# Kernel optimization log

Measured on AMD Instinct MI355X. Metric: run time of the kernel, lower is better.

## Reference

```python
import jax, jax.numpy as jnp
import numpy as np

N, E, G, H, IN = 50000, 500000, 64, 128, 5
BN_EPS = 1e-5


def setup_inputs() -> dict:
    key = jax.random.key(0)
    ks = jax.random.split(key, 12)
    x = jax.random.normal(ks[0], (N, IN), dtype=jnp.float32)
    edge_index = jax.random.randint(ks[1], (2, E), 0, N, dtype=jnp.int64)
    edge_attr = jax.random.uniform(ks[2], (E,), dtype=jnp.float32)
    batch = jnp.sort(jax.random.randint(ks[3], (N,), 0, G, dtype=jnp.int64))
    conv0_w = jax.random.normal(ks[4], (IN, H), dtype=jnp.float32) / np.sqrt(IN)
    conv0_b = jnp.zeros((H,), jnp.float32)
    conv_ws = jax.random.normal(ks[5], (3, H, H), dtype=jnp.float32) / np.sqrt(H)
    conv_bs = jnp.zeros((3, H), jnp.float32)
    bn_gamma = jnp.ones((4, H), jnp.float32)
    bn_beta = jnp.zeros((4, H), jnp.float32)
    fc1_w = jax.random.normal(ks[6], (H, 64), dtype=jnp.float32) / np.sqrt(H)
    fc1_b = jnp.zeros((64,), jnp.float32)
    fc2_w = jax.random.normal(ks[7], (64, 1), dtype=jnp.float32) / np.sqrt(64)
    fc2_b = jnp.zeros((1,), jnp.float32)
    return dict(x=x, edge_index=edge_index, edge_attr=edge_attr, batch=batch,
                num_graphs=G, conv0_w=conv0_w, conv0_b=conv0_b, conv_ws=conv_ws,
                conv_bs=conv_bs, bn_gamma=bn_gamma, bn_beta=bn_beta,
                fc1_w=fc1_w, fc1_b=fc1_b, fc2_w=fc2_w, fc2_b=fc2_b)


def reference(x, edge_index, edge_attr, batch, num_graphs, conv0_w, conv0_b,
              conv_ws, conv_bs, bn_gamma, bn_beta, fc1_w, fc1_b, fc2_w, fc2_b):
    n = x.shape[0]
    row, col = edge_index[0], edge_index[1]
    # PyG gcn_norm: add self-loops (weight 1), symmetric D^-1/2 A D^-1/2
    loops = jnp.arange(n)
    row_f = jnp.concatenate([row, loops])
    col_f = jnp.concatenate([col, loops])
    ew = jnp.concatenate([edge_attr, jnp.ones((n,), x.dtype)])
    deg = jax.ops.segment_sum(ew, col_f, num_segments=n)
    dinv = jnp.where(deg > 0, jax.lax.rsqrt(jnp.where(deg > 0, deg, 1.0)), 0.0)
    norm = dinv[row_f] * ew * dinv[col_f]  # [E+N]

    def gcn_conv(h, W, b):
        m = h @ W  # transform first, as in PyG GCNConv
        agg = jax.ops.segment_sum(norm[:, None] * m[row_f], col_f, num_segments=n)
        return agg + b

    def bn(h, g, bta):  # training-mode BatchNorm1d, biased variance
        mu = h.mean(axis=0)
        var = jnp.mean((h - mu) ** 2, axis=0)
        return g * (h - mu) * jax.lax.rsqrt(var + BN_EPS) + bta

    h = jax.nn.silu(bn(gcn_conv(x, conv0_w, conv0_b), bn_gamma[0], bn_beta[0]))
    for i in range(3):
        h = jax.nn.silu(bn(gcn_conv(h, conv_ws[i], conv_bs[i]),
                           bn_gamma[i + 1], bn_beta[i + 1]))

    # global_mean_pool over graph ids
    sums = jax.ops.segment_sum(h, batch, num_segments=num_graphs)
    counts = jax.ops.segment_sum(jnp.ones((n,), h.dtype), batch, num_segments=num_graphs)
    pooled = sums / jnp.maximum(counts, 1.0)[:, None]

    out = jax.nn.silu(pooled @ fc1_w + fc1_b)
    out = jax.nn.sigmoid(out @ fc2_w + fc2_b)
    return out
```

## Files before the change

### kernel.cpp

```cpp
#include <hip/hip_runtime.h>

#define NN 50000
#define NE 500000
#define NGR 64
#define HD 128
#define INF 5
#define BN_EPS 1e-5f
#define BM 64
#define SCB 128
#define SCT 256
#define SCH ((NN + SCB - 1) / SCB)
#define PP 16
#define NWFU (3 * 8 * 4 * 64 * 4)
#define PAD8(c) (((c) + 7) & ~7)

typedef __attribute__((ext_vector_type(8))) short short8v;
typedef __attribute__((ext_vector_type(4))) float f32x4;

__device__ __forceinline__ float bflo(unsigned u) { return __uint_as_float(u << 16); }
__device__ __forceinline__ float bfhi(unsigned u) { return __uint_as_float(u & 0xffff0000u); }
__device__ __forceinline__ unsigned bfpack(float a, float b) {
    unsigned ua = __float_as_uint(a), ub = __float_as_uint(b);
    ua = (ua + 0x7fffu + ((ua >> 16) & 1u)) >> 16;
    ub = (ub + 0x7fffu + ((ub >> 16) & 1u)) >> 16;
    return ua | (ub << 16);
}
__device__ __forceinline__ unsigned short bf1(float a) {
    unsigned ua = __float_as_uint(a);
    return (unsigned short)((ua + 0x7fffu + ((ua >> 16) & 1u)) >> 16);
}

__global__ void k_init(int* fill, float* stats, const float* __restrict__ conv_ws,
                       unsigned* __restrict__ wbf) {
    int i = blockIdx.x * 256 + threadIdx.x;
    if (i < NN) fill[i] = 0;
    if (i < 4 * 2 * HD) stats[i] = 0.f;
    if (i < NWFU) {
        int inner = i & 3;
        int u4 = i >> 2;
        int lane = u4 & 63;
        int rest = u4 >> 6;
        int s = rest & 3, tt = (rest >> 2) & 7, L = rest >> 5;
        int col = tt * 16 + (lane & 15);
        int k = s * 32 + (lane >> 4) * 8 + inner * 2;
        const float* Wl = conv_ws + (size_t)L * HD * HD;
        wbf[i] = bfpack(Wl[k * HD + col], Wl[(k + 1) * HD + col]);
    }
}

__global__ void k_pos(const int* __restrict__ ei, int* __restrict__ fill,
                      int* __restrict__ pos) {
    int e = blockIdx.x * 256 + threadIdx.x;
    if (e < NE) pos[e] = atomicAdd(&fill[ei[NE + e]], 1);
}

__global__ void k_scan1(const int* __restrict__ cnt, int* __restrict__ bsum) {
    __shared__ int sm[SCT];
    int b = blockIdx.x, t = threadIdx.x;
    int lo = b * SCH, hi = min(lo + SCH, NN);
    int s = 0;
    for (int i = lo + t; i < hi; i += SCT) s += PAD8(cnt[i]);
    sm[t] = s;
    __syncthreads();
    for (int off = SCT / 2; off > 0; off >>= 1) {
        if (t < off) sm[t] += sm[t + off];
        __syncthreads();
    }
    if (t == 0) bsum[b] = sm[0];
}

__global__ void k_scan2_gb(const int* __restrict__ bsum, int* __restrict__ boff,
                           const int* __restrict__ batch, int* __restrict__ gstart) {
    int t = threadIdx.x;
    if (blockIdx.x == 1) {
        int g = t;
        if (g > NGR) return;
        int lo = 0, hi = NN;
        while (lo < hi) {
            int mid = (lo + hi) >> 1;
            if (batch[mid] < g) lo = mid + 1;
            else hi = mid;
        }
        gstart[g] = lo;
        return;
    }
    __shared__ int sm[SCB];
    sm[t] = bsum[t];
    __syncthreads();
    for (int off = 1; off < SCB; off <<= 1) {
        int v = (t >= off) ? sm[t - off] : 0;
        __syncthreads();
        sm[t] += v;
        __syncthreads();
    }
    boff[t] = (t == 0) ? 0 : sm[t - 1];
    if (t == SCB - 1) boff[SCB] = sm[SCB - 1];
}

__global__ void k_scan3(const int* __restrict__ cnt, const int* __restrict__ boff,
                        int* __restrict__ col_ptr) {
    __shared__ int sm[SCT];
    int b = blockIdx.x, t = threadIdx.x;
    int lo = b * SCH, hi = min(lo + SCH, NN);
    int e0 = lo + 2 * t, e1 = e0 + 1;
    int c0 = (e0 < hi) ? PAD8(cnt[e0]) : 0;
    int c1 = (e1 < hi) ? PAD8(cnt[e1]) : 0;
    sm[t] = c0 + c1;
    __syncthreads();
    for (int off = 1; off < SCT; off <<= 1) {
        int v = (t >= off) ? sm[t - off] : 0;
        __syncthreads();
        sm[t] += v;
        __syncthreads();
    }
    int base = boff[b] + ((t == 0) ? 0 : sm[t - 1]);
    if (e0 < hi) col_ptr[e0] = base;
    if (e1 < hi) col_ptr[e1] = base + c0;
    if (b == SCB - 1 && t == SCT - 1) col_ptr[NN] = boff[SCB];
}

__global__ void k_scatter(const int* __restrict__ ei, const float* __restrict__ ea,
                          const int* __restrict__ col_ptr, const int* __restrict__ pos,
                          int2* __restrict__ sw) {
    int e = blockIdx.x * 256 + threadIdx.x;
    if (e >= NE) return;
    int c = ei[NE + e];
    int p = col_ptr[c] + pos[e];
    sw[p] = make_int2(ei[e], __float_as_int(ea[e]));
}

__global__ void k_degsum(const int* __restrict__ col_ptr, const int* __restrict__ cnt,
                         int2* __restrict__ sw, float* __restrict__ dinv) {
    int i = blockIdx.x * 256 + threadIdx.x;
    if (i >= NN) return;
    int beg = col_ptr[i], mid = beg + cnt[i], end = col_ptr[i + 1];
    float s = 1.0f;
    for (int p = beg; p < mid; p++) s += __int_as_float(sw[p].y);
    for (int p = mid; p < end; p++) sw[p] = make_int2(0, 0);
    dinv[i] = rsqrtf(s);
}

__global__ void k_gemm0(const float* __restrict__ x, const float* __restrict__ W,
                        unsigned* __restrict__ m32) {
    __shared__ float Ws[INF][HD];
    int t = threadIdx.x;
    for (int i = t; i < INF * HD; i += 256) ((float*)Ws)[i] = W[i];
    __syncthreads();
    int row = blockIdx.x * 4 + (t >> 6);
    if (row >= NN) return;
    int lane = t & 63;
    int c0 = 2 * lane;
    float xv[INF];
#pragma unroll
    for (int k = 0; k < INF; k++) xv[k] = x[row * INF + k];
    float a0 = 0.f, a1 = 0.f;
#pragma unroll
    for (int k = 0; k < INF; k++) {
        a0 += xv[k] * Ws[k][c0];
        a1 += xv[k] * Ws[k][c0 + 1];
    }
    m32[(size_t)row * 64 + lane] = bfpack(a0, a1);
}

__global__ __launch_bounds__(256) void k_gemm128(
    const unsigned* __restrict__ h32, const float* __restrict__ stats,
    const float* __restrict__ gamma, const float* __restrict__ beta,
    const uint4* __restrict__ wfrag, unsigned short* __restrict__ m16) {
    __shared__ __align__(16) unsigned hs[64 * 64];
    __shared__ float sc[HD], sh[HD];
    int t = threadIdx.x;
    int r0 = blockIdx.x * BM;
    const float invn = 1.0f / NN;

    if (t < HD) {
        float mu = stats[t] * invn;
        float var = stats[HD + t] * invn - mu * mu;
        float s = gamma[t] * rsqrtf(var + BN_EPS);
        sc[t] = s;
        sh[t] = beta[t] - mu * s;
    }
    __syncthreads();

#pragma unroll
    for (int j = 0; j < 8; j++) {
        int g = j * 256 + t;
        int r = g >> 5;
        int u2 = g & 31;
        uint2 v = make_uint2(0u, 0u);
        if (r0 + r < NN) v = ((const uint2*)h32)[(size_t)(r0 + r) * 32 + u2];
        int c = u2 * 4;
        float y0 = sc[c] * bflo(v.x) + sh[c];
        float y1 = sc[c + 1] * bfhi(v.x) + sh[c + 1];
        float y2 = sc[c + 2] * bflo(v.y) + sh[c + 2];
        float y3 = sc[c + 3] * bfhi(v.y) + sh[c + 3];
        y0 = y0 / (1.f + __expf(-y0));
        y1 = y1 / (1.f + __expf(-y1));
        y2 = y2 / (1.f + __expf(-y2));
        y3 = y3 / (1.f + __expf(-y3));
        int slot = u2 >> 1, inner = (u2 & 1) * 2;
        int addr = r * 64 + ((slot ^ (r & 7)) << 2) + inner;
        hs[addr] = bfpack(y0, y1);
        hs[addr + 1] = bfpack(y2, y3);
    }
    __syncthreads();

    int w = t >> 6, l = t & 63;
    int lr = l & 15, lg = l >> 4;
    f32x4 acc[8];
#pragma unroll
    for (int i = 0; i < 8; i++) acc[i] = (f32x4){0.f, 0.f, 0.f, 0.f};

#pragma unroll
    for (int s = 0; s < 4; s++) {
        int arow = w * 16 + lr;
        int q = s * 4 + lg;
        short8v af = *reinterpret_cast<const short8v*>(
            &hs[arow * 64 + ((q ^ (arow & 7)) << 2)]);
#pragma unroll
        for (int tt = 0; tt < 8; tt++) {
            short8v bf = *reinterpret_cast<const short8v*>(&wfrag[(tt * 4 + s) * 64 + l]);
            acc[tt] = __builtin_amdgcn_mfma_f32_16x16x32_bf16(af, bf, acc[tt], 0, 0, 0);
        }
    }

    int baserow = r0 + w * 16 + lg * 4;
#pragma unroll
    for (int tt = 0; tt < 8; tt++) {
        int col = tt * 16 + lr;
#pragma unroll
        for (int reg = 0; reg < 4; reg++) {
            int row = baserow + reg;
            if (row < NN) m16[(size_t)row * HD + col] = bf1(acc[tt][reg]);
        }
    }
}

template <bool NORM>
__global__ void k_agg(const unsigned* __restrict__ m32, const int* __restrict__ col_ptr,
                      int2* __restrict__ sw, const float* __restrict__ dinv,
                      const float* __restrict__ bias, unsigned* __restrict__ hpre32) {
    int node = blockIdx.x * 4 + (threadIdx.x >> 6);
    if (node >= NN) return;
    int lane = threadIdx.x & 63;
    float di = dinv[node];
    unsigned sv = m32[(size_t)node * 64 + lane];
    float a0 = di * di * bflo(sv);
    float a1 = di * di * bfhi(sv);
    int beg = col_ptr[node], end = col_ptr[node + 1];
    for (int p = beg; p < end; p += 8) {
        int2 e0 = sw[p], e1 = sw[p + 1], e2 = sw[p + 2], e3 = sw[p + 3];
        int2 e4 = sw[p + 4], e5 = sw[p + 5], e6 = sw[p + 6], e7 = sw[p + 7];
        int s0 = __builtin_amdgcn_readfirstlane(e0.x);
        int s1 = __builtin_amdgcn_readfirstlane(e1.x);
        int s2 = __builtin_amdgcn_readfirstlane(e2.x);
        int s3 = __builtin_amdgcn_readfirstlane(e3.x);
        int s4 = __builtin_amdgcn_readfirstlane(e4.x);
        int s5 = __builtin_amdgcn_readfirstlane(e5.x);
        int s6 = __builtin_amdgcn_readfirstlane(e6.x);
        int s7 = __builtin_amdgcn_readfirstlane(e7.x);
        unsigned v0 = m32[(size_t)s0 * 64 + lane];
        unsigned v1 = m32[(size_t)s1 * 64 + lane];
        unsigned v2 = m32[(size_t)s2 * 64 + lane];
        unsigned v3 = m32[(size_t)s3 * 64 + lane];
        unsigned v4 = m32[(size_t)s4 * 64 + lane];
        unsigned v5 = m32[(size_t)s5 * 64 + lane];
        unsigned v6 = m32[(size_t)s6 * 64 + lane];
        unsigned v7 = m32[(size_t)s7 * 64 + lane];
        float w0 = __int_as_float(__builtin_amdgcn_readfirstlane(e0.y));
        float w1 = __int_as_float(__builtin_amdgcn_readfirstlane(e1.y));
        float w2 = __int_as_float(__builtin_amdgcn_readfirstlane(e2.y));
        float w3 = __int_as_float(__builtin_amdgcn_readfirstlane(e3.y));
        float w4 = __int_as_float(__builtin_amdgcn_readfirstlane(e4.y));
        float w5 = __int_as_float(__builtin_amdgcn_readfirstlane(e5.y));
        float w6 = __int_as_float(__builtin_amdgcn_readfirstlane(e6.y));
        float w7 = __int_as_float(__builtin_amdgcn_readfirstlane(e7.y));
        if (NORM) {
            w0 = dinv[s0] * w0 * di;
            w1 = dinv[s1] * w1 * di;
            w2 = dinv[s2] * w2 * di;
            w3 = dinv[s3] * w3 * di;
            w4 = dinv[s4] * w4 * di;
            w5 = dinv[s5] * w5 * di;
            w6 = dinv[s6] * w6 * di;
            w7 = dinv[s7] * w7 * di;
            if (lane == 0) {
                sw[p].y = __float_as_int(w0);
                sw[p + 1].y = __float_as_int(w1);
                sw[p + 2].y = __float_as_int(w2);
                sw[p + 3].y = __float_as_int(w3);
                sw[p + 4].y = __float_as_int(w4);
                sw[p + 5].y = __float_as_int(w5);
                sw[p + 6].y = __float_as_int(w6);
                sw[p + 7].y = __float_as_int(w7);
            }
        }
        a0 += w0 * bflo(v0) + w1 * bflo(v1) + w2 * bflo(v2) + w3 * bflo(v3);
        a1 += w0 * bfhi(v0) + w1 * bfhi(v1) + w2 * bfhi(v2) + w3 * bfhi(v3);
        a0 += w4 * bflo(v4) + w5 * bflo(v5) + w6 * bflo(v6) + w7 * bflo(v7);
        a1 += w4 * bfhi(v4) + w5 * bfhi(v5) + w6 * bfhi(v6) + w7 * bfhi(v7);
    }
    float2 b = ((const float2*)bias)[lane];
    hpre32[(size_t)node * 64 + lane] = bfpack(a0 + b.x, a1 + b.y);
}

__global__ void k_bnstats(const unsigned* __restrict__ h32, float* __restrict__ stats) {
    __shared__ float lss[4][HD];
    __shared__ float lsq[4][HD];
    int t = threadIdx.x;
    int w = t >> 6, l = t & 63;
    float s0 = 0.f, s1 = 0.f, q0 = 0.f, q1 = 0.f;
    for (int r = blockIdx.x * 4 + w; r < NN; r += 1024) {
        unsigned v = h32[(size_t)r * 64 + l];
        float a = bflo(v), b = bfhi(v);
        s0 += a; q0 += a * a;
        s1 += b; q1 += b * b;
    }
    lss[w][2 * l] = s0;
    lss[w][2 * l + 1] = s1;
    lsq[w][2 * l] = q0;
    lsq[w][2 * l + 1] = q1;
    __syncthreads();
    if (t < HD) {
        float s = lss[0][t] + lss[1][t] + lss[2][t] + lss[3][t];
        atomicAdd(&stats[t], s);
    } else {
        int c = t - HD;
        float q = lsq[0][c] + lsq[1][c] + lsq[2][c] + lsq[3][c];
        atomicAdd(&stats[HD + c], q);
    }
}

__global__ void k_poolp(const unsigned* __restrict__ h32, const float* __restrict__ stats,
                        const float* __restrict__ gamma, const float* __restrict__ beta,
                        const int* __restrict__ gstart, float* __restrict__ ppool) {
    int g = blockIdx.x / PP, p = blockIdx.x % PP;
    int t = threadIdx.x;
    int c4 = t & 31;
    int ro = t >> 5;
    const float invn = 1.0f / NN;
    float sc[4], sh[4];
#pragma unroll
    for (int q = 0; q < 4; q++) {
        int c = c4 * 4 + q;
        float mu = stats[c] * invn;
        float var = stats[HD + c] * invn - mu * mu;
        float s = gamma[c] * rsqrtf(var + BN_EPS);
        sc[q] = s;
        sh[q] = beta[c] - mu * s;
    }
    int beg = gstart[g], end = gstart[g + 1];
    const uint2* h2 = (const uint2*)h32;
    float4 acc = make_float4(0.f, 0.f, 0.f, 0.f);
    for (int r = beg + p * 8 + ro; r < end; r += PP * 8) {
        uint2 u = h2[(size_t)r * 32 + c4];
        float vals[4] = {bflo(u.x), bfhi(u.x), bflo(u.y), bfhi(u.y)};
#pragma unroll
        for (int q = 0; q < 4; q++) {
            float y = sc[q] * vals[q] + sh[q];
            (&acc.x)[q] += y / (1.f + __expf(-y));
        }
    }
    __shared__ float4 sm[256];
    sm[t] = acc;
    __syncthreads();
    if (t < 128) {
        float4 o = sm[t + 128];
        sm[t].x += o.x; sm[t].y += o.y; sm[t].z += o.z; sm[t].w += o.w;
    }
    __syncthreads();
    if (t < 64) {
        float4 o = sm[t + 64];
        sm[t].x += o.x; sm[t].y += o.y; sm[t].z += o.z; sm[t].w += o.w;
    }
    __syncthreads();
    if (t < 32) {
        float4 o = sm[t + 32];
        float4 r = sm[t];
        r.x += o.x; r.y += o.y; r.z += o.z; r.w += o.w;
        ((float4*)ppool)[(size_t)blockIdx.x * 32 + t] = r;
    }
}

__global__ void k_pool_head(const float* __restrict__ ppool, const int* __restrict__ gstart,
                            const float* __restrict__ fc1w, const float* __restrict__ fc1b,
                            const float* __restrict__ fc2w, const float* __restrict__ fc2b,
                            float* __restrict__ out) {
    int g = blockIdx.x;
    int t = threadIdx.x;
    __shared__ float pa[HD];
    float s = 0.f;
    for (int p = 0; p < PP; p++) s += ppool[(size_t)(g * PP + p) * HD + t];
    float cnt = (float)(gstart[g + 1] - gstart[g]);
    pa[t] = s / fmaxf(cnt, 1.0f);
    __syncthreads();
    if (t < 64) {
        float a = fc1b[t];
        for (int k = 0; k < HD; k++) a += pa[k] * fc1w[k * 64 + t];
        a = a / (1.f + __expf(-a));
        float v = a * fc2w[t];
        for (int off = 32; off > 0; off >>= 1) v += __shfl_down(v, off);
        if (t == 0) out[g] = 1.f / (1.f + __expf(-(v + fc2b[0])));
    }
}

extern "C" void kernel_launch(void* const* d_in, const int* in_sizes, int n_in,
                              void* d_out, int out_size, void* d_ws, size_t ws_size,
                              hipStream_t stream) {
    const float* x = (const float*)d_in[0];
    const int* ei = (const int*)d_in[1];
    const float* ea = (const float*)d_in[2];
    const int* batch = (const int*)d_in[3];
    const float* conv0_w = (const float*)d_in[5];
    const float* conv0_b = (const float*)d_in[6];
    const float* conv_ws = (const float*)d_in[7];
    const float* conv_bs = (const float*)d_in[8];
    const float* bn_gamma = (const float*)d_in[9];
    const float* bn_beta = (const float*)d_in[10];
    const float* fc1w = (const float*)d_in[11];
    const float* fc1b = (const float*)d_in[12];
    const float* fc2w = (const float*)d_in[13];
    const float* fc2b = (const float*)d_in[14];
    float* out = (float*)d_out;

    char* ws = (char*)d_ws;
    size_t off = 0;
    auto alloc = [&](size_t bytes) -> char* {
        char* p = ws + off;
        off = (off + bytes + 255) & ~(size_t)255;
        return p;
    };
    float* dinv = (float*)alloc(NN * 4);
    int* fill = (int*)alloc(NN * 4);
    int* col_ptr = (int*)alloc((NN + 1) * 4);
    int* pos = (int*)alloc(NE * 4);
    int2* sw = (int2*)alloc(((size_t)NE + 8 * NN) * 8);
    unsigned* mbuf = (unsigned*)alloc((size_t)NN * HD * 2);
    unsigned* hA = (unsigned*)alloc((size_t)NN * HD * 2);
    unsigned* hB = (unsigned*)alloc((size_t)NN * HD * 2);
    unsigned* wbf = (unsigned*)alloc((size_t)NWFU * 4);
    float* stats = (float*)alloc(4 * 2 * HD * 4);
    float* ppool = (float*)alloc((size_t)NGR * PP * HD * 4);
    int* gstart = (int*)alloc((NGR + 1) * 4);
    int* bsum = (int*)alloc(SCB * 4);
    int* boff = (int*)alloc((SCB + 1) * 4);

    k_init<<<(NN + 255) / 256, 256, 0, stream>>>(fill, stats, conv_ws, wbf);
    k_pos<<<(NE + 255) / 256, 256, 0, stream>>>(ei, fill, pos);
    k_scan1<<<SCB, SCT, 0, stream>>>(fill, bsum);
    k_scan2_gb<<<2, SCB, 0, stream>>>(bsum, boff, batch, gstart);
    k_scan3<<<SCB, SCT, 0, stream>>>(fill, boff, col_ptr);
    k_scatter<<<(NE + 255) / 256, 256, 0, stream>>>(ei, ea, col_ptr, pos, sw);
    k_degsum<<<(NN + 255) / 256, 256, 0, stream>>>(col_ptr, fill, sw, dinv);

    float* st0 = stats;
    float* st1 = stats + 2 * HD;
    float* st2 = stats + 4 * HD;
    float* st3 = stats + 6 * HD;
    const int NG128 = (NN + BM - 1) / BM;
    const uint4* wf = (const uint4*)wbf;

    k_gemm0<<<(NN + 3) / 4, 256, 0, stream>>>(x, conv0_w, mbuf);
    k_agg<true><<<(NN + 3) / 4, 256, 0, stream>>>(mbuf, col_ptr, sw, dinv, conv0_b, hA);
    k_bnstats<<<256, 256, 0, stream>>>(hA, st0);
    k_gemm128<<<NG128, 256, 0, stream>>>(hA, st0, bn_gamma, bn_beta, wf,
                                         (unsigned short*)mbuf);
    k_agg<false><<<(NN + 3) / 4, 256, 0, stream>>>(mbuf, col_ptr, sw, dinv, conv_bs, hB);
    k_bnstats<<<256, 256, 0, stream>>>(hB, st1);
    k_gemm128<<<NG128, 256, 0, stream>>>(hB, st1, bn_gamma + HD, bn_beta + HD, wf + 2048,
                                         (unsigned short*)mbuf);
    k_agg<false><<<(NN + 3) / 4, 256, 0, stream>>>(mbuf, col_ptr, sw, dinv, conv_bs + HD, hA);
    k_bnstats<<<256, 256, 0, stream>>>(hA, st2);
    k_gemm128<<<NG128, 256, 0, stream>>>(hA, st2, bn_gamma + 2 * HD, bn_beta + 2 * HD,
                                         wf + 4096, (unsigned short*)mbuf);
    k_agg<false><<<(NN + 3) / 4, 256, 0, stream>>>(mbuf, col_ptr, sw, dinv,
                                                   conv_bs + 2 * HD, hB);
    k_bnstats<<<256, 256, 0, stream>>>(hB, st3);
    k_poolp<<<NGR * PP, 256, 0, stream>>>(hB, st3, bn_gamma + 3 * HD, bn_beta + 3 * HD,
                                          gstart, ppool);
    k_pool_head<<<NGR, HD, 0, stream>>>(ppool, gstart, fc1w, fc1b, fc2w, fc2b, out);
}
```

Before: 302.9 us.

## Fuse BatchNorm statistics into aggregation kernel with persistent grid-stride waves

Removes the separate k_bnstats pass by accumulating per-channel sums and sums of squares of the rounded bf16 outputs inside k_agg. Each wave reduces into shared memory and then issues atomics. The aggregation kernel becomes a persistent grid-stride launch of 512 blocks of 1024 threads, each wave looping over nodes. This saves four launches and four full re-reads of the hidden activations, at the cost of a fixed grid that may balance load less well and higher per-block resource pressure.

```diff
diff --git a/kernel.cpp b/kernel.cpp
--- a/kernel.cpp
+++ b/kernel.cpp
@@ -13,6 +13,8 @@
 #define PP 16
 #define NWFU (3 * 8 * 4 * 64 * 4)
 #define PAD8(c) (((c) + 7) & ~7)
+#define AGB 512
+#define AGW (AGB * 16)
 
 typedef __attribute__((ext_vector_type(8))) short short8v;
 typedef __attribute__((ext_vector_type(4))) float f32x4;
@@ -236,96 +238,99 @@
 }
 
 template <bool NORM>
-__global__ void k_agg(const unsigned* __restrict__ m32, const int* __restrict__ col_ptr,
-                      int2* __restrict__ sw, const float* __restrict__ dinv,
-                      const float* __restrict__ bias, unsigned* __restrict__ hpre32) {
-    int node = blockIdx.x * 4 + (threadIdx.x >> 6);
-    if (node >= NN) return;
-    int lane = threadIdx.x & 63;
-    float di = dinv[node];
-    unsigned sv = m32[(size_t)node * 64 + lane];
-    float a0 = di * di * bflo(sv);
-    float a1 = di * di * bfhi(sv);
-    int beg = col_ptr[node], end = col_ptr[node + 1];
-    for (int p = beg; p < end; p += 8) {
-        int2 e0 = sw[p], e1 = sw[p + 1], e2 = sw[p + 2], e3 = sw[p + 3];
-        int2 e4 = sw[p + 4], e5 = sw[p + 5], e6 = sw[p + 6], e7 = sw[p + 7];
-        int s0 = __builtin_amdgcn_readfirstlane(e0.x);
-        int s1 = __builtin_amdgcn_readfirstlane(e1.x);
-        int s2 = __builtin_amdgcn_readfirstlane(e2.x);
-        int s3 = __builtin_amdgcn_readfirstlane(e3.x);
-        int s4 = __builtin_amdgcn_readfirstlane(e4.x);
-        int s5 = __builtin_amdgcn_readfirstlane(e5.x);
-        int s6 = __builtin_amdgcn_readfirstlane(e6.x);
-        int s7 = __builtin_amdgcn_readfirstlane(e7.x);
-        unsigned v0 = m32[(size_t)s0 * 64 + lane];
-        unsigned v1 = m32[(size_t)s1 * 64 + lane];
-        unsigned v2 = m32[(size_t)s2 * 64 + lane];
-        unsigned v3 = m32[(size_t)s3 * 64 + lane];
-        unsigned v4 = m32[(size_t)s4 * 64 + lane];
-        unsigned v5 = m32[(size_t)s5 * 64 + lane];
-        unsigned v6 = m32[(size_t)s6 * 64 + lane];
-        unsigned v7 = m32[(size_t)s7 * 64 + lane];
-        float w0 = __int_as_float(__builtin_amdgcn_readfirstlane(e0.y));
-        float w1 = __int_as_float(__builtin_amdgcn_readfirstlane(e1.y));
-        float w2 = __int_as_float(__builtin_amdgcn_readfirstlane(e2.y));
-        float w3 = __int_as_float(__builtin_amdgcn_readfirstlane(e3.y));
-        float w4 = __int_as_float(__builtin_amdgcn_readfirstlane(e4.y));
-        float w5 = __int_as_float(__builtin_amdgcn_readfirstlane(e5.y));
-        float w6 = __int_as_float(__builtin_amdgcn_readfirstlane(e6.y));
-        float w7 = __int_as_float(__builtin_amdgcn_readfirstlane(e7.y));
-        if (NORM) {
-            w0 = dinv[s0] * w0 * di;
-            w1 = dinv[s1] * w1 * di;
-            w2 = dinv[s2] * w2 * di;
-            w3 = dinv[s3] * w3 * di;
-            w4 = dinv[s4] * w4 * di;
-            w5 = dinv[s5] * w5 * di;
-            w6 = dinv[s6] * w6 * di;
-            w7 = dinv[s7] * w7 * di;
-            if (lane == 0) {
-                sw[p].y = __float_as_int(w0);
-                sw[p + 1].y = __float_as_int(w1);
-                sw[p + 2].y = __float_as_int(w2);
-                sw[p + 3].y = __float_as_int(w3);
-                sw[p + 4].y = __float_as_int(w4);
-                sw[p + 5].y = __float_as_int(w5);
-                sw[p + 6].y = __float_as_int(w6);
-                sw[p + 7].y = __float_as_int(w7);
+__global__ __launch_bounds__(1024, 8) void k_agg(
+    const unsigned* __restrict__ m32, const int* __restrict__ col_ptr,
+    int2* __restrict__ sw, const float* __restrict__ dinv,
+    const float* __restrict__ bias, unsigned* __restrict__ hpre32,
+    float* __restrict__ stats) {
+    int t = threadIdx.x;
+    int w = t >> 6, lane = t & 63;
+    int gwave = blockIdx.x * 16 + w;
+    float2 b = ((const float2*)bias)[lane];
+    float ss0 = 0.f, ss1 = 0.f, sq0 = 0.f, sq1 = 0.f;
+
+    for (int node = gwave; node < NN; node += AGW) {
+        float di = dinv[node];
+        unsigned sv = m32[(size_t)node * 64 + lane];
+        float a0 = di * di * bflo(sv);
+        float a1 = di * di * bfhi(sv);
+        int beg = col_ptr[node], end = col_ptr[node + 1];
+        for (int p = beg; p < end; p += 8) {
+            int2 e0 = sw[p], e1 = sw[p + 1], e2 = sw[p + 2], e3 = sw[p + 3];
+            int2 e4 = sw[p + 4], e5 = sw[p + 5], e6 = sw[p + 6], e7 = sw[p + 7];
+            int s0 = __builtin_amdgcn_readfirstlane(e0.x);
+            int s1 = __builtin_amdgcn_readfirstlane(e1.x);
+            int s2 = __builtin_amdgcn_readfirstlane(e2.x);
+            int s3 = __builtin_amdgcn_readfirstlane(e3.x);
+            int s4 = __builtin_amdgcn_readfirstlane(e4.x);
+            int s5 = __builtin_amdgcn_readfirstlane(e5.x);
+            int s6 = __builtin_amdgcn_readfirstlane(e6.x);
+            int s7 = __builtin_amdgcn_readfirstlane(e7.x);
+            unsigned v0 = m32[(size_t)s0 * 64 + lane];
+            unsigned v1 = m32[(size_t)s1 * 64 + lane];
+            unsigned v2 = m32[(size_t)s2 * 64 + lane];
+            unsigned v3 = m32[(size_t)s3 * 64 + lane];
+            unsigned v4 = m32[(size_t)s4 * 64 + lane];
+            unsigned v5 = m32[(size_t)s5 * 64 + lane];
+            unsigned v6 = m32[(size_t)s6 * 64 + lane];
+            unsigned v7 = m32[(size_t)s7 * 64 + lane];
+            float w0 = __int_as_float(__builtin_amdgcn_readfirstlane(e0.y));
+            float w1 = __int_as_float(__builtin_amdgcn_readfirstlane(e1.y));
+            float w2 = __int_as_float(__builtin_amdgcn_readfirstlane(e2.y));
+            float w3 = __int_as_float(__builtin_amdgcn_readfirstlane(e3.y));
+            float w4 = __int_as_float(__builtin_amdgcn_readfirstlane(e4.y));
+            float w5 = __int_as_float(__builtin_amdgcn_readfirstlane(e5.y));
+            float w6 = __int_as_float(__builtin_amdgcn_readfirstlane(e6.y));
+            float w7 = __int_as_float(__builtin_amdgcn_readfirstlane(e7.y));
+            if (NORM) {
+                w0 = dinv[s0] * w0 * di;
+                w1 = dinv[s1] * w1 * di;
+                w2 = dinv[s2] * w2 * di;
+                w3 = dinv[s3] * w3 * di;
+                w4 = dinv[s4] * w4 * di;
+                w5 = dinv[s5] * w5 * di;
+                w6 = dinv[s6] * w6 * di;
+                w7 = dinv[s7] * w7 * di;
+                if (lane == 0) {
+                    sw[p].y = __float_as_int(w0);
+                    sw[p + 1].y = __float_as_int(w1);
+                    sw[p + 2].y = __float_as_int(w2);
+                    sw[p + 3].y = __float_as_int(w3);
+                    sw[p + 4].y = __float_as_int(w4);
+                    sw[p + 5].y = __float_as_int(w5);
+                    sw[p + 6].y = __float_as_int(w6);
+                    sw[p + 7].y = __float_as_int(w7);
+                }
             }
+            a0 += w0 * bflo(v0) + w1 * bflo(v1) + w2 * bflo(v2) + w3 * bflo(v3);
+            a1 += w0 * bfhi(v0) + w1 * bfhi(v1) + w2 * bfhi(v2) + w3 * bfhi(v3);
+            a0 += w4 * bflo(v4) + w5 * bflo(v5) + w6 * bflo(v6) + w7 * bflo(v7);
+            a1 += w4 * bfhi(v4) + w5 * bfhi(v5) + w6 * bfhi(v6) + w7 * bfhi(v7);
         }
-        a0 += w0 * bflo(v0) + w1 * bflo(v1) + w2 * bflo(v2) + w3 * bflo(v3);
-        a1 += w0 * bfhi(v0) + w1 * bfhi(v1) + w2 * bfhi(v2) + w3 * bfhi(v3);
-        a0 += w4 * bflo(v4) + w5 * bflo(v5) + w6 * bflo(v6) + w7 * bflo(v7);
-        a1 += w4 * bfhi(v4) + w5 * bfhi(v5) + w6 * bfhi(v6) + w7 * bfhi(v7);
-    }
-    float2 b = ((const float2*)bias)[lane];
-    hpre32[(size_t)node * 64 + lane] = bfpack(a0 + b.x, a1 + b.y);
-}
-
-__global__ void k_bnstats(const unsigned* __restrict__ h32, float* __restrict__ stats) {
-    __shared__ float lss[4][HD];
-    __shared__ float lsq[4][HD];
-    int t = threadIdx.x;
-    int w = t >> 6, l = t & 63;
-    float s0 = 0.f, s1 = 0.f, q0 = 0.f, q1 = 0.f;
-    for (int r = blockIdx.x * 4 + w; r < NN; r += 1024) {
-        unsigned v = h32[(size_t)r * 64 + l];
-        float a = bflo(v), b = bfhi(v);
-        s0 += a; q0 += a * a;
-        s1 += b; q1 += b * b;
-    }
-    lss[w][2 * l] = s0;
-    lss[w][2 * l + 1] = s1;
-    lsq[w][2 * l] = q0;
-    lsq[w][2 * l + 1] = q1;
+        unsigned pk = bfpack(a0 + b.x, a1 + b.y);
+        hpre32[(size_t)node * 64 + lane] = pk;
+        float r0 = bflo(pk), r1 = bfhi(pk);
+        ss0 += r0; sq0 += r0 * r0;
+        ss1 += r1; sq1 += r1 * r1;
+    }
+
+    __shared__ float lsum[16][HD];
+    __shared__ float lsqr[16][HD];
+    lsum[w][2 * lane] = ss0;
+    lsum[w][2 * lane + 1] = ss1;
+    lsqr[w][2 * lane] = sq0;
+    lsqr[w][2 * lane + 1] = sq1;
     __syncthreads();
     if (t < HD) {
-        float s = lss[0][t] + lss[1][t] + lss[2][t] + lss[3][t];
+        float s = 0.f;
+#pragma unroll
+        for (int i = 0; i < 16; i++) s += lsum[i][t];
         atomicAdd(&stats[t], s);
-    } else {
+    } else if (t < 2 * HD) {
         int c = t - HD;
-        float q = lsq[0][c] + lsq[1][c] + lsq[2][c] + lsq[3][c];
+        float q = 0.f;
+#pragma unroll
+        for (int i = 0; i < 16; i++) q += lsqr[i][c];
         atomicAdd(&stats[HD + c], q);
     }
 }
@@ -460,21 +465,17 @@
     const uint4* wf = (const uint4*)wbf;
 
     k_gemm0<<<(NN + 3) / 4, 256, 0, stream>>>(x, conv0_w, mbuf);
-    k_agg<true><<<(NN + 3) / 4, 256, 0, stream>>>(mbuf, col_ptr, sw, dinv, conv0_b, hA);
-    k_bnstats<<<256, 256, 0, stream>>>(hA, st0);
+    k_agg<true><<<AGB, 1024, 0, stream>>>(mbuf, col_ptr, sw, dinv, conv0_b, hA, st0);
     k_gemm128<<<NG128, 256, 0, stream>>>(hA, st0, bn_gamma, bn_beta, wf,
                                          (unsigned short*)mbuf);
-    k_agg<false><<<(NN + 3) / 4, 256, 0, stream>>>(mbuf, col_ptr, sw, dinv, conv_bs, hB);
-    k_bnstats<<<256, 256, 0, stream>>>(hB, st1);
+    k_agg<false><<<AGB, 1024, 0, stream>>>(mbuf, col_ptr, sw, dinv, conv_bs, hB, st1);
     k_gemm128<<<NG128, 256, 0, stream>>>(hB, st1, bn_gamma + HD, bn_beta + HD, wf + 2048,
                                          (unsigned short*)mbuf);
-    k_agg<false><<<(NN + 3) / 4, 256, 0, stream>>>(mbuf, col_ptr, sw, dinv, conv_bs + HD, hA);
-    k_bnstats<<<256, 256, 0, stream>>>(hA, st2);
+    k_agg<false><<<AGB, 1024, 0, stream>>>(mbuf, col_ptr, sw, dinv, conv_bs + HD, hA, st2);
     k_gemm128<<<NG128, 256, 0, stream>>>(hA, st2, bn_gamma + 2 * HD, bn_beta + 2 * HD,
                                          wf + 4096, (unsigned short*)mbuf);
-    k_agg<false><<<(NN + 3) / 4, 256, 0, stream>>>(mbuf, col_ptr, sw, dinv,
-                                                   conv_bs + 2 * HD, hB);
-    k_bnstats<<<256, 256, 0, stream>>>(hB, st3);
+    k_agg<false><<<AGB, 1024, 0, stream>>>(mbuf, col_ptr, sw, dinv, conv_bs + 2 * HD, hB,
+                                           st3);
     k_poolp<<<NGR * PP, 256, 0, stream>>>(hB, st3, bn_gamma + 3 * HD, bn_beta + 3 * HD,
                                           gstart, ppool);
     k_pool_head<<<NGR, HD, 0, stream>>>(ppool, gstart, fc1w, fc1b, fc2w, fc2b, out);
```

Measured after the change: 268.1 us. -11.5%, faster.
